# Kernel optimization log

Measured on AMD Instinct MI355X. Metric: run time of the kernel, lower is better.

Reference implementation:

```python
import jax, jax.numpy as jnp
import numpy as np

NEG_INF = -1e9

def setup_inputs() -> dict:
    key = jax.random.key(0)
    kq, kk, kv, kt, km = jax.random.split(key, 5)
    B, H, S, D = 2, 16, 2048, 64
    query = jax.random.normal(kq, (B, H, S, D), dtype=jnp.float32)
    k_ = jax.random.normal(kk, (B, H, S, D), dtype=jnp.float32)
    value = jax.random.normal(kv, (B, H, S, D), dtype=jnp.float32)
    time = jax.random.normal(kt, (B, H, S, D), dtype=jnp.float32)
    mask = jax.random.randint(km, (B, 1, S, S), 0, 2, dtype=jnp.int32)
    return {"query": query, "key": k_, "value": value, "time": time, "mask": mask}

def reference(query, key, value, time, mask):
    # scores = (Q K^T + Q T^T) / sqrt(D)  == Q (K+T)^T / sqrt(D)
    scale = 1.0 / jnp.sqrt(jnp.asarray(query.shape[-1], query.dtype))
    query_time = jnp.einsum('bhqd,bhkd->bhqk', query, time) * scale
    query_key = jnp.einsum('bhqd,bhkd->bhqk', query, key) * scale
    scores = query_time + query_key
    scores = jnp.where(mask == 0, jnp.asarray(NEG_INF, scores.dtype), scores)
    p_attn = jax.nn.softmax(scores, axis=-1)
    out = jnp.einsum('bhqk,bhkd->bhqd', p_attn, value)
    return (out, p_attn)
```

## Files before the change

kernel.cpp:

```cpp
#include <hip/hip_runtime.h>
#include <hip/hip_bf16.h>

#define TA_B 2
#define TA_H 16
#define TA_S 2048
#define TA_D 64
#define KTILE 64
#define QB 128
#define BLOCK 512
#define NKT (TA_S / KTILE)

typedef __attribute__((ext_vector_type(4))) float f32x4;
typedef __attribute__((ext_vector_type(8))) short bf16x8;
typedef __attribute__((ext_vector_type(8))) unsigned short u16x8;
typedef __attribute__((ext_vector_type(4))) unsigned short u16x4;

union BF8 { u16x8 u; bf16x8 s; };

__device__ __forceinline__ unsigned short f2bf(float f) {
    union { float f; unsigned int i; } v; v.f = f;
    unsigned int x = v.i;
    unsigned int r = x + 0x7FFFu + ((x >> 16) & 1u);
    return (unsigned short)(r >> 16);
}
__device__ __forceinline__ float bf2f(unsigned short u) {
    union { unsigned int i; float f; } v; v.i = ((unsigned int)u) << 16; return v.f;
}

__device__ __forceinline__ void barrier_lds() {
    asm volatile("s_waitcnt lgkmcnt(0)" ::: "memory");
    __builtin_amdgcn_sched_barrier(0);
    __builtin_amdgcn_s_barrier();
    __builtin_amdgcn_sched_barrier(0);
}

__global__ __launch_bounds__(256) void pack_mask(const int* __restrict__ M,
                                                 unsigned long long* __restrict__ Mp) {
    const int nw = TA_B * TA_S * NKT;
    const int wavesTotal = (gridDim.x * blockDim.x) >> 6;
    const int wid  = (blockIdx.x * blockDim.x + threadIdx.x) >> 6;
    const int lane = threadIdx.x & 63;
    for (int w = wid; w < nw; w += wavesTotal) {
        int mv = M[(long)w * 64 + lane];
        unsigned long long bits = __ballot(mv != 0);
        if (lane == 0) Mp[w] = bits;
    }
}

template <bool PACKED>
__global__ __launch_bounds__(BLOCK, 4) void ta_fused(
    const float* __restrict__ Qg,
    const float* __restrict__ Kg,
    const float* __restrict__ Vg,
    const float* __restrict__ Tg,
    const int* __restrict__ Mg,
    const unsigned long long* __restrict__ Mp,
    float* __restrict__ Og,
    float* __restrict__ Pg)
{
    __shared__ unsigned short sKp[2][KTILE][72];
    __shared__ unsigned short sVt[2][TA_D][72];
    __shared__ unsigned short sP[QB][72];

    const int tid  = threadIdx.x;
    const int wave = tid >> 6;
    const int lane = tid & 63;
    const int c    = lane & 15;
    const int g    = lane >> 4;
    const int row0 = tid >> 3;
    const int cg   = (tid & 7) * 8;

    const int did = blockIdx.x + 16 * (blockIdx.y + 16 * blockIdx.z);
    const int wid = (did & 7) * 64 + (did >> 3);
    const int q0  = (wid & 15) * QB;
    const int h   = (wid >> 4) & 15;
    const int b   = wid >> 8;

    const long bh    = (long)b * TA_H + h;
    const long xBase = bh * (long)TA_S * TA_D;
    const long pBase = bh * (long)TA_S * TA_S;
    const long mBase = (long)b * (long)TA_S * TA_S;
    const int  wq0   = wave * 16;

    bf16x8 qf0, qf1;
    {
        const float* qp = Qg + xBase + (long)(q0 + wq0 + c) * TA_D + g * 8;
        f32x4 a0 = *(const f32x4*)(qp);
        f32x4 a1 = *(const f32x4*)(qp + 4);
        f32x4 b0 = *(const f32x4*)(qp + 32);
        f32x4 b1 = *(const f32x4*)(qp + 36);
        BF8 u0, u1;
#pragma unroll
        for (int i = 0; i < 4; ++i) {
            u0.u[i]     = f2bf(a0[i] * 0.125f);
            u0.u[i + 4] = f2bf(a1[i] * 0.125f);
            u1.u[i]     = f2bf(b0[i] * 0.125f);
            u1.u[i + 4] = f2bf(b1[i] * 0.125f);
        }
        qf0 = u0.s; qf1 = u1.s;
    }

    f32x4 kA0, kA1, tA0, tA1, vA0, vA1;

    auto loadKT = [&](int kt) {
        const long o0 = xBase + (long)(kt * KTILE + row0) * TA_D + cg;
        kA0 = *(const f32x4*)(Kg + o0); kA1 = *(const f32x4*)(Kg + o0 + 4);
        tA0 = *(const f32x4*)(Tg + o0); tA1 = *(const f32x4*)(Tg + o0 + 4);
    };
    auto loadV = [&](int kt) {
        const long o0 = xBase + (long)(kt * KTILE + row0) * TA_D + cg;
        vA0 = *(const f32x4*)(Vg + o0); vA1 = *(const f32x4*)(Vg + o0 + 4);
    };
    auto storeKp = [&](int p) {
        u16x8 r0;
#pragma unroll
        for (int i = 0; i < 4; ++i) {
            r0[i]     = f2bf(kA0[i] + tA0[i]);
            r0[i + 4] = f2bf(kA1[i] + tA1[i]);
        }
        *(u16x8*)&sKp[p][row0][cg] = r0;
    };
    auto storeVt = [&](int p) {
        const int kp = row0 ^ cg;
#pragma unroll
        for (int i = 0; i < 4; ++i) {
            sVt[p][cg + i][kp]     = f2bf(vA0[i]);
            sVt[p][cg + i + 4][kp] = f2bf(vA1[i]);
        }
    };

    auto maskBits = [&](int kt, int r, float* mb) {
        const int mq = q0 + wq0 + g * 4 + r;
        if constexpr (PACKED) {
            const unsigned long long w = Mp[((long)b * TA_S + mq) * NKT + kt];
            const unsigned lo = (unsigned)w, hi = (unsigned)(w >> 32);
            mb[0] = ((lo >> c) & 1u)        ? 1.0f : 0.0f;
            mb[1] = ((lo >> (16 + c)) & 1u) ? 1.0f : 0.0f;
            mb[2] = ((hi >> c) & 1u)        ? 1.0f : 0.0f;
            mb[3] = ((hi >> (16 + c)) & 1u) ? 1.0f : 0.0f;
        } else {
            const int* mp = Mg + mBase + (long)mq * TA_S + kt * KTILE;
#pragma unroll
            for (int ct = 0; ct < 4; ++ct) mb[ct] = mp[ct * 16 + c] ? 1.0f : 0.0f;
        }
    };

    float lpart[4] = {0.0f, 0.0f, 0.0f, 0.0f};
    loadKT(0);
    for (int kt = 0; kt < NKT; ++kt) {
        const int p = kt & 1;
        storeKp(p);
        loadKT(kt + 1 < NKT ? kt + 1 : 0);
        barrier_lds();

        f32x4 acc[4];
#pragma unroll
        for (int ct = 0; ct < 4; ++ct)
#pragma unroll
            for (int j = 0; j < 4; ++j) acc[ct][j] = 0.0f;

        __builtin_amdgcn_s_setprio(1);
#pragma unroll
        for (int kk = 0; kk < 2; ++kk) {
            bf16x8 qa = kk ? qf1 : qf0;
#pragma unroll
            for (int ct = 0; ct < 4; ++ct) {
                BF8 bf; bf.u = *(const u16x8*)&sKp[p][ct * 16 + c][kk * 32 + g * 8];
                acc[ct] = __builtin_amdgcn_mfma_f32_16x16x32_bf16(qa, bf.s, acc[ct], 0, 0, 0);
            }
        }
        __builtin_amdgcn_s_setprio(0);

#pragma unroll
        for (int r = 0; r < 4; ++r) {
            float mb[4];
            maskBits(kt, r, mb);
#pragma unroll
            for (int ct = 0; ct < 4; ++ct)
                lpart[r] += mb[ct] * __expf(acc[ct][r]);
        }
    }

    loadV(0);

    float invl[4];
#pragma unroll
    for (int r = 0; r < 4; ++r) {
        float l = lpart[r];
#pragma unroll
        for (int off = 1; off < 16; off <<= 1)
            l += __shfl_xor(l, off);
        invl[r] = (l > 0.0f) ? (1.0f / l) : 0.0f;
    }

    f32x4 oacc[4];
#pragma unroll
    for (int dt = 0; dt < 4; ++dt)
#pragma unroll
        for (int j = 0; j < 4; ++j) oacc[dt][j] = 0.0f;

    for (int kt = 0; kt < NKT; ++kt) {
        const int p = kt & 1;
        storeKp(p);
        storeVt(p);
        const int ktn = kt + 1 < NKT ? kt + 1 : 0;
        loadKT(ktn);
        loadV(ktn);
        barrier_lds();

        f32x4 acc[4];
#pragma unroll
        for (int ct = 0; ct < 4; ++ct)
#pragma unroll
            for (int j = 0; j < 4; ++j) acc[ct][j] = 0.0f;

        __builtin_amdgcn_s_setprio(1);
#pragma unroll
        for (int kk = 0; kk < 2; ++kk) {
            bf16x8 qa = kk ? qf1 : qf0;
#pragma unroll
            for (int ct = 0; ct < 4; ++ct) {
                BF8 bf; bf.u = *(const u16x8*)&sKp[p][ct * 16 + c][kk * 32 + g * 8];
                acc[ct] = __builtin_amdgcn_mfma_f32_16x16x32_bf16(qa, bf.s, acc[ct], 0, 0, 0);
            }
        }
        __builtin_amdgcn_s_setprio(0);

#pragma unroll
        for (int r = 0; r < 4; ++r) {
            float mb[4];
            maskBits(kt, r, mb);
#pragma unroll
            for (int ct = 0; ct < 4; ++ct) {
                float e = mb[ct] * __expf(acc[ct][r]);
                sP[wq0 + g * 4 + r][((ct ^ r) << 4) + c] = f2bf(e * invl[r]);
            }
        }

        BF8 pa0, pa1;
        {
            const int m = c & 3;
            pa0.u = *(const u16x8*)&sP[wq0 + c][(((g >> 1) ^ m) << 4) + ((g & 1) << 3)];
            pa1.u = *(const u16x8*)&sP[wq0 + c][(((2 | (g >> 1)) ^ m) << 4) + ((g & 1) << 3)];
        }
        __builtin_amdgcn_s_setprio(1);
#pragma unroll
        for (int dt = 0; dt < 4; ++dt) {
            const int dRow = dt * 16 + c;
            const int kc0 = (g * 8) ^ (dRow & 56);
            const int kc1 = (32 + g * 8) ^ (dRow & 56);
            BF8 bv0, bv1;
            bv0.u = *(const u16x8*)&sVt[p][dRow][kc0];
            oacc[dt] = __builtin_amdgcn_mfma_f32_16x16x32_bf16(pa0.s, bv0.s, oacc[dt], 0, 0, 0);
            bv1.u = *(const u16x8*)&sVt[p][dRow][kc1];
            oacc[dt] = __builtin_amdgcn_mfma_f32_16x16x32_bf16(pa1.s, bv1.s, oacc[dt], 0, 0, 0);
        }
        __builtin_amdgcn_s_setprio(0);

#pragma unroll
        for (int j = 0; j < 4; ++j) {
            const int prow = 4 * j + (g & 3);
            const int L0   = c * 4;
            const int phys = (L0 & 12) + ((((L0 >> 4) ^ (prow & 3)) << 4));
            u16x4 pv = *(const u16x4*)&sP[wq0 + prow][phys];
            f32x4 v;
#pragma unroll
            for (int i = 0; i < 4; ++i) v[i] = bf2f(pv[i]);
            __builtin_nontemporal_store(
                v, (f32x4*)(Pg + pBase + (long)(q0 + wq0 + prow) * TA_S + kt * KTILE + L0));
        }
    }

#pragma unroll
    for (int dt = 0; dt < 4; ++dt) {
#pragma unroll
        for (int r = 0; r < 4; ++r) {
            __builtin_nontemporal_store(
                oacc[dt][r],
                &Og[xBase + (long)(q0 + wq0 + g * 4 + r) * TA_D + dt * 16 + c]);
        }
    }
}

extern "C" void kernel_launch(void* const* d_in, const int* in_sizes, int n_in,
                              void* d_out, int out_size, void* d_ws, size_t ws_size,
                              hipStream_t stream) {
    const float* Q = (const float*)d_in[0];
    const float* K = (const float*)d_in[1];
    const float* V = (const float*)d_in[2];
    const float* T = (const float*)d_in[3];
    const int*   M = (const int*)d_in[4];

    float* O = (float*)d_out;
    float* P = O + (long)TA_B * TA_H * TA_S * TA_D;

    unsigned long long* Mp = (unsigned long long*)d_ws;
    const size_t needWs = (size_t)TA_B * TA_S * NKT * sizeof(unsigned long long);

    dim3 grid(TA_S / QB, TA_H, TA_B);
    dim3 block(BLOCK);

    if (ws_size >= needWs) {
        hipLaunchKernelGGL(pack_mask, dim3(512), dim3(256), 0, stream, M, Mp);
        hipLaunchKernelGGL(ta_fused<true>, grid, block, 0, stream, Q, K, V, T, M, Mp, O, P);
    } else {
        hipLaunchKernelGGL(ta_fused<false>, grid, block, 0, stream, Q, K, V, T, M, Mp, O, P);
    }
}
```

Baseline: 193.3 us.

## Transpose QK MFMA so lanes own query rows; store P directly from registers

Swaps the MFMA operand order so each lane holds four consecutive key columns of a single query row. The mask then becomes one 64-bit word per lane per tile, and the row sum needs only two shuffles. P is written to global memory directly from fp32 registers, so the readback from the LDS P tile and the bf16-to-fp32 conversion go away. P is also stored exactly in fp32 rather than as bf16-rounded values. The LDS writes of P now use 8-byte stores without an XOR swizzle, which may cause bank conflicts.

```diff
diff --git a/kernel.cpp b/kernel.cpp
--- a/kernel.cpp
+++ b/kernel.cpp
@@ -13,7 +13,7 @@
 typedef __attribute__((ext_vector_type(4))) float f32x4;
 typedef __attribute__((ext_vector_type(8))) short bf16x8;
 typedef __attribute__((ext_vector_type(8))) unsigned short u16x8;
-typedef __attribute__((ext_vector_type(4))) unsigned short u16x4;
+typedef __attribute__((ext_vector_type(2))) unsigned int u32x2;
 
 union BF8 { u16x8 u; bf16x8 s; };
 
@@ -22,9 +22,6 @@
     unsigned int x = v.i;
     unsigned int r = x + 0x7FFFu + ((x >> 16) & 1u);
     return (unsigned short)(r >> 16);
-}
-__device__ __forceinline__ float bf2f(unsigned short u) {
-    union { unsigned int i; float f; } v; v.i = ((unsigned int)u) << 16; return v.f;
 }
 
 __device__ __forceinline__ void barrier_lds() {
@@ -81,10 +78,11 @@
     const long pBase = bh * (long)TA_S * TA_S;
     const long mBase = (long)b * (long)TA_S * TA_S;
     const int  wq0   = wave * 16;
+    const int  myq   = q0 + wq0 + c;
 
     bf16x8 qf0, qf1;
     {
-        const float* qp = Qg + xBase + (long)(q0 + wq0 + c) * TA_D + g * 8;
+        const float* qp = Qg + xBase + (long)myq * TA_D + g * 8;
         f32x4 a0 = *(const f32x4*)(qp);
         f32x4 a1 = *(const f32x4*)(qp + 4);
         f32x4 b0 = *(const f32x4*)(qp + 32);
@@ -129,23 +127,22 @@
         }
     };
 
-    auto maskBits = [&](int kt, int r, float* mb) {
-        const int mq = q0 + wq0 + g * 4 + r;
+    auto maskWord = [&](int kt) -> unsigned long long {
         if constexpr (PACKED) {
-            const unsigned long long w = Mp[((long)b * TA_S + mq) * NKT + kt];
-            const unsigned lo = (unsigned)w, hi = (unsigned)(w >> 32);
-            mb[0] = ((lo >> c) & 1u)        ? 1.0f : 0.0f;
-            mb[1] = ((lo >> (16 + c)) & 1u) ? 1.0f : 0.0f;
-            mb[2] = ((hi >> c) & 1u)        ? 1.0f : 0.0f;
-            mb[3] = ((hi >> (16 + c)) & 1u) ? 1.0f : 0.0f;
+            return Mp[((long)b * TA_S + myq) * NKT + kt];
         } else {
-            const int* mp = Mg + mBase + (long)mq * TA_S + kt * KTILE;
-#pragma unroll
-            for (int ct = 0; ct < 4; ++ct) mb[ct] = mp[ct * 16 + c] ? 1.0f : 0.0f;
-        }
-    };
-
-    float lpart[4] = {0.0f, 0.0f, 0.0f, 0.0f};
+            const int* mp = Mg + mBase + (long)myq * TA_S + kt * KTILE;
+            unsigned long long w = 0;
+#pragma unroll
+            for (int ct = 0; ct < 4; ++ct)
+#pragma unroll
+                for (int r = 0; r < 4; ++r)
+                    w |= mp[ct * 16 + g * 4 + r] ? (1ull << (ct * 16 + g * 4 + r)) : 0ull;
+            return w;
+        }
+    };
+
+    float lpart = 0.0f;
     loadKT(0);
     for (int kt = 0; kt < NKT; ++kt) {
         const int p = kt & 1;
@@ -166,32 +163,27 @@
 #pragma unroll
             for (int ct = 0; ct < 4; ++ct) {
                 BF8 bf; bf.u = *(const u16x8*)&sKp[p][ct * 16 + c][kk * 32 + g * 8];
-                acc[ct] = __builtin_amdgcn_mfma_f32_16x16x32_bf16(qa, bf.s, acc[ct], 0, 0, 0);
+                acc[ct] = __builtin_amdgcn_mfma_f32_16x16x32_bf16(bf.s, qa, acc[ct], 0, 0, 0);
             }
         }
         __builtin_amdgcn_s_setprio(0);
 
-#pragma unroll
-        for (int r = 0; r < 4; ++r) {
-            float mb[4];
-            maskBits(kt, r, mb);
-#pragma unroll
-            for (int ct = 0; ct < 4; ++ct)
-                lpart[r] += mb[ct] * __expf(acc[ct][r]);
+        const unsigned long long w = maskWord(kt);
+#pragma unroll
+        for (int ct = 0; ct < 4; ++ct) {
+            const unsigned nib = (unsigned)(w >> (ct * 16 + g * 4)) & 0xFu;
+#pragma unroll
+            for (int r = 0; r < 4; ++r)
+                lpart += ((nib >> r) & 1u) ? __expf(acc[ct][r]) : 0.0f;
         }
     }
 
     loadV(0);
 
-    float invl[4];
-#pragma unroll
-    for (int r = 0; r < 4; ++r) {
-        float l = lpart[r];
-#pragma unroll
-        for (int off = 1; off < 16; off <<= 1)
-            l += __shfl_xor(l, off);
-        invl[r] = (l > 0.0f) ? (1.0f / l) : 0.0f;
-    }
+    float l = lpart;
+    l += __shfl_xor(l, 16);
+    l += __shfl_xor(l, 32);
+    const float invl = (l > 0.0f) ? (1.0f / l) : 0.0f;
 
     f32x4 oacc[4];
 #pragma unroll
@@ -221,28 +213,32 @@
 #pragma unroll
             for (int ct = 0; ct < 4; ++ct) {
                 BF8 bf; bf.u = *(const u16x8*)&sKp[p][ct * 16 + c][kk * 32 + g * 8];
-                acc[ct] = __builtin_amdgcn_mfma_f32_16x16x32_bf16(qa, bf.s, acc[ct], 0, 0, 0);
+                acc[ct] = __builtin_amdgcn_mfma_f32_16x16x32_bf16(bf.s, qa, acc[ct], 0, 0, 0);
             }
         }
         __builtin_amdgcn_s_setprio(0);
 
-#pragma unroll
-        for (int r = 0; r < 4; ++r) {
-            float mb[4];
-            maskBits(kt, r, mb);
-#pragma unroll
-            for (int ct = 0; ct < 4; ++ct) {
-                float e = mb[ct] * __expf(acc[ct][r]);
-                sP[wq0 + g * 4 + r][((ct ^ r) << 4) + c] = f2bf(e * invl[r]);
+        const unsigned long long w = maskWord(kt);
+        float* prow = Pg + pBase + (long)myq * TA_S + kt * KTILE;
+#pragma unroll
+        for (int ct = 0; ct < 4; ++ct) {
+            const unsigned nib = (unsigned)(w >> (ct * 16 + g * 4)) & 0xFu;
+            f32x4 pv;
+#pragma unroll
+            for (int r = 0; r < 4; ++r) {
+                float e = ((nib >> r) & 1u) ? __expf(acc[ct][r]) : 0.0f;
+                pv[r] = e * invl;
             }
+            __builtin_nontemporal_store(pv, (f32x4*)(prow + ct * 16 + g * 4));
+            u32x2 pk;
+            pk[0] = (unsigned)f2bf(pv[0]) | ((unsigned)f2bf(pv[1]) << 16);
+            pk[1] = (unsigned)f2bf(pv[2]) | ((unsigned)f2bf(pv[3]) << 16);
+            *(u32x2*)&sP[wq0 + c][ct * 16 + g * 4] = pk;
         }
 
         BF8 pa0, pa1;
-        {
-            const int m = c & 3;
-            pa0.u = *(const u16x8*)&sP[wq0 + c][(((g >> 1) ^ m) << 4) + ((g & 1) << 3)];
-            pa1.u = *(const u16x8*)&sP[wq0 + c][(((2 | (g >> 1)) ^ m) << 4) + ((g & 1) << 3)];
-        }
+        pa0.u = *(const u16x8*)&sP[wq0 + c][g * 8];
+        pa1.u = *(const u16x8*)&sP[wq0 + c][32 + g * 8];
         __builtin_amdgcn_s_setprio(1);
 #pragma unroll
         for (int dt = 0; dt < 4; ++dt) {
@@ -256,19 +252,6 @@
             oacc[dt] = __builtin_amdgcn_mfma_f32_16x16x32_bf16(pa1.s, bv1.s, oacc[dt], 0, 0, 0);
         }
         __builtin_amdgcn_s_setprio(0);
-
-#pragma unroll
-        for (int j = 0; j < 4; ++j) {
-            const int prow = 4 * j + (g & 3);
-            const int L0   = c * 4;
-            const int phys = (L0 & 12) + ((((L0 >> 4) ^ (prow & 3)) << 4));
-            u16x4 pv = *(const u16x4*)&sP[wq0 + prow][phys];
-            f32x4 v;
-#pragma unroll
-            for (int i = 0; i < 4; ++i) v[i] = bf2f(pv[i]);
-            __builtin_nontemporal_store(
-                v, (f32x4*)(Pg + pBase + (long)(q0 + wq0 + prow) * TA_S + kt * KTILE + L0));
-        }
     }
 
 #pragma unroll
```

New measurement: 220.9 us. +14.3%, slower.
